# Optimization experiments

Hardware: AMD Instinct MI355X
Metric: run time of the kernel (lower is better)

The kernel has to match this reference:

```python
import jax, jax.numpy as jnp
import numpy as np

P, F, FR = 288, 7, 12      # time slots per day, days per week, sampling frequency scale
CHEB_K = 2
HID = 64


def _ste(time_index, SE, W_se, b_se, T_tod, T_dow):
    """Spatio-temporal embedding: learned spatial embedding projected to et_dim,
    plus time-of-day and day-of-week temporal embeddings. -> [B, N, et]"""
    t = time_index * FR
    tod = T_tod[t % P]                 # [B, et]
    dow = T_dow[(t // P) % F]          # [B, et]
    se = SE @ W_se + b_se              # [N, et]
    return se[None, :, :] + (tod + dow)[:, None, :]


def _avwgcn(x, STE, R, SC, Wpool, bpool):
    """Adaptive-vertex-weight graph conv (AGCRN-style) with dynamic STE-driven
    adjacency blended with dynamic relation R and static correlation SC.
    x: [B,N,Cin], STE: [B,N,et], R: [B,N,N], SC: [N,N]."""
    A = jax.nn.softmax(
        jax.nn.relu(jnp.einsum('bnd,bmd->bnm', STE, STE)) + R + SC[None], axis=-1)
    # Chebyshev polynomial supports applied to x (T0 = I handled implicitly)
    xs = [x, jnp.einsum('bnm,bmc->bnc', A, x)]
    for _ in range(CHEB_K - 2):
        xs.append(2.0 * jnp.einsum('bnm,bmc->bnc', A, xs[-1]) - xs[-2])
    x_g = jnp.stack(xs, axis=2)                        # [B,N,K,Cin]
    # per-node adaptive weights: W_n = STE @ Wpool; contracted without
    # materializing the [B,N,K,Cin,Cout] tensor
    g = jnp.einsum('bnki,dkio->bndo', x_g, Wpool)      # [B,N,et,Cout]
    out = jnp.einsum('bndo,bnd->bno', g, STE) + jnp.einsum('bnd,do->bno', STE, bpool)
    return out


def setup_inputs() -> dict:
    key = jax.random.key(0)
    ks = jax.random.split(key, 12)
    B, N, Din, et, es = 32, 1024, 1, 16, 16
    std = 0.1
    return {
        "x": jax.random.normal(ks[0], (B, N, Din), jnp.float32),
        "R": jax.random.normal(ks[1], (B, N, N), jnp.float32) * std,
        "state": jax.random.normal(ks[2], (B, N, HID), jnp.float32),
        "SC": jax.random.normal(ks[3], (N, N), jnp.float32) * std,
        "SE": jax.random.normal(ks[4], (N, es), jnp.float32),
        "W_se": jax.random.normal(ks[5], (es, et), jnp.float32) * std,
        "b_se": jnp.zeros((et,), jnp.float32),
        "T_tod": jax.random.normal(ks[6], (P, et), jnp.float32) * std,
        "T_dow": jax.random.normal(ks[7], (F, et), jnp.float32) * std,
        "W_gate": jax.random.normal(ks[8], (et, CHEB_K, Din + HID, 2 * HID), jnp.float32) * std,
        "b_gate": jnp.zeros((et, 2 * HID), jnp.float32),
        "W_upd": jax.random.normal(ks[9], (et, CHEB_K, Din + HID, HID), jnp.float32) * std,
        "b_upd": jnp.zeros((et, HID), jnp.float32),
        "time_index": jax.random.randint(ks[10], (B,), 0, P * F),
    }


def reference(x, R, state, SC, SE, W_se, b_se, T_tod, T_dow,
              W_gate, b_gate, W_upd, b_upd, time_index):
    STE = _ste(time_index, SE, W_se, b_se, T_tod, T_dow)       # [B,N,et]
    ins = jnp.concatenate([x, state], axis=-1)                 # [B,N,Din+H]
    z_r = jax.nn.sigmoid(_avwgcn(ins, STE, R, SC, W_gate, b_gate))
    z, r = jnp.split(z_r, 2, axis=-1)                          # each [B,N,H]
    cand = jnp.concatenate([x, z * state], axis=-1)
    hc = jnp.tanh(_avwgcn(cand, STE, R, SC, W_upd, b_upd))
    return r * state + (1.0 - r) * hc                          # [B,N,H]
```

## Files before the change

### kernel.cpp

```cpp
#include <hip/hip_runtime.h>
#include <math.h>

namespace {
constexpr int BB = 32;
constexpr int NN = 1024;
constexpr int ET = 16;
constexpr int HH = 64;
constexpr int CIN = 65;
constexpr int KI = 2*CIN;
constexpr int COG = 2*HH;
constexpr int COU = HH;
constexpr int PP = 288;
constexpr int FF = 7;
constexpr int FRQ = 12;
constexpr int XK = 160;

typedef __attribute__((ext_vector_type(4))) float f32x4;
typedef __attribute__((ext_vector_type(8))) short s16x8;
typedef __attribute__((ext_vector_type(4))) unsigned int u32x4;
typedef unsigned long long ull;

__device__ __forceinline__ float bf2f(unsigned short u) {
    unsigned v = ((unsigned)u) << 16;
    return __builtin_bit_cast(float, v);
}
__device__ __forceinline__ unsigned short f2bf(float f) {
    unsigned u = __builtin_bit_cast(unsigned, f);
    u += 0x7fffu + ((u >> 16) & 1u);
    return (unsigned short)(u >> 16);
}
__device__ __forceinline__ unsigned cvtpk(float lo, float hi) {
    unsigned r;
    asm("v_cvt_pk_bf16_f32 %0, %1, %2" : "=v"(r) : "v"(lo), "v"(hi));
    return r;
}
__device__ __forceinline__ float ldany(const float* p) { return *p; }
__device__ __forceinline__ float ldany(const unsigned short* p) { return bf2f(*p); }

__global__ void k_prep1(const float* __restrict__ SE, const float* __restrict__ Wse,
                        const float* __restrict__ bse, const float* __restrict__ Ttod,
                        const float* __restrict__ Tdow, const int* __restrict__ tidx,
                        float* __restrict__ se, float* __restrict__ tt) {
    int idx = blockIdx.x*blockDim.x + threadIdx.x;
    if (idx < NN*ET) {
        int n = idx / ET, d = idx % ET;
        float acc = bse[d];
        #pragma unroll
        for (int e = 0; e < ET; ++e) acc += SE[n*ET + e]*Wse[e*ET + d];
        se[idx] = acc;
    } else if (idx < NN*ET + BB*ET) {
        int r = idx - NN*ET;
        int b = r / ET, d = r % ET;
        int t = tidx[b]*FRQ;
        tt[r] = Ttod[(t % PP)*ET + d] + Tdow[((t/PP) % FF)*ET + d];
    }
}

__global__ void k_prep2(const float* __restrict__ se, const float* __restrict__ tt,
                        const float* __restrict__ Wg, const float* __restrict__ Wu,
                        unsigned short* __restrict__ stebf,
                        unsigned short* __restrict__ Wptg, unsigned short* __restrict__ Wptu) {
    int idx = blockIdx.x*blockDim.x + threadIdx.x;
    if (idx < BB*NN*ET) {
        int d = idx % ET;
        int n = (idx/ET) % NN;
        int b = idx/(ET*NN);
        stebf[idx] = f2bf(se[n*ET+d] + tt[b*ET+d]);
        return;
    }
    idx -= BB*NN*ET;
    if (idx < ET*COG*XK) {
        int d = idx/(COG*XK), r = idx%(COG*XK), o = r/XK, ki = r%XK;
        float v = (ki < KI) ? Wg[((size_t)d*KI + ki)*COG + o] : 0.f;
        Wptg[((size_t)d*COG + o)*XK + ki] = f2bf(v);
        return;
    }
    idx -= ET*COG*XK;
    if (idx < ET*COU*XK) {
        int d = idx/(COU*XK), r = idx%(COU*XK), o = r/XK, ki = r%XK;
        float v = (ki < KI) ? Wu[((size_t)d*KI + ki)*COU + o] : 0.f;
        Wptu[((size_t)d*COU + o)*XK + ki] = f2bf(v);
    }
}

template<typename T>
__global__ void k_vin(const float* __restrict__ x, const T* __restrict__ sv,
                      unsigned short* __restrict__ xgbf, unsigned short* __restrict__ vt) {
    int idx = blockIdx.x*blockDim.x + threadIdx.x;
    if (idx < BB*128*64) {
        int och = idx & 63, mb = (idx >> 6) & 127, b = idx >> 13;
        const T* src = sv + ((size_t)b*NN + mb*8)*HH + och;
        float v0=ldany(src), v1=ldany(src+HH), v2=ldany(src+2*HH), v3=ldany(src+3*HH);
        float v4=ldany(src+4*HH), v5=ldany(src+5*HH), v6=ldany(src+6*HH), v7=ldany(src+7*HH);
        ull lo = (ull)f2bf(v0) | ((ull)f2bf(v1)<<16) | ((ull)f2bf(v2)<<32) | ((ull)f2bf(v3)<<48);
        ull hi = (ull)f2bf(v4) | ((ull)f2bf(v5)<<16) | ((ull)f2bf(v6)<<32) | ((ull)f2bf(v7)<<48);
        ull* dst = (ull*)(vt + (size_t)idx*8);
        dst[0] = lo; dst[1] = hi;
        return;
    }
    idx -= BB*128*64;
    if (idx >= BB*NN*(XK/2)) return;
    int row = idx/(XK/2), c = idx%(XK/2);
    if (c < 32) {
        int k0 = 2*c;
        float v0 = (k0 == 0) ? x[row] : ldany(sv + (size_t)row*HH + k0 - 1);
        float v1 = ldany(sv + (size_t)row*HH + k0);
        ((unsigned*)xgbf)[(size_t)row*(XK/2) + c] = ((unsigned)f2bf(v1) << 16) | f2bf(v0);
    } else if (c == 32) {
        xgbf[(size_t)row*XK + 64] = f2bf(ldany(sv + (size_t)row*HH + 63));
    } else if (c >= 65) {
        ((unsigned*)xgbf)[(size_t)row*(XK/2) + c] = 0;
    }
}

constexpr int SSTR   = 1048;
constexpr int S_OFF  = 0;
constexpr int XV_OFF = 33536;
constexpr int MSH_OFF  = 37632;
constexpr int MSHC_OFF = 37888;
constexpr int LP_OFF   = 37952;
constexpr int AXP_OFF  = 38208;
constexpr int LSH_OFF  = 38464;
constexpr int SMEM_BYTES = 38528;

template<int PASS>
__global__ __launch_bounds__(256, 4) void k_attn(
    const unsigned short* __restrict__ stebf, const float* __restrict__ Rg,
    const float* __restrict__ SCg, const float* __restrict__ xg,
    const unsigned short* __restrict__ vt,
    float* __restrict__ Mr, float* __restrict__ Li,
    unsigned short* __restrict__ xgout, unsigned short* __restrict__ pglob)
{
    extern __shared__ char smem[];
    const int t = threadIdx.x, lane = t & 63, w = t >> 6;
    const int c15 = lane & 15, g = lane >> 4;
    const int strip = blockIdx.x, b = blockIdx.y;
    const size_t bN = (size_t)b * NN;
    const int r0 = strip * 16;

    float* Mshf  = (float*)(smem + MSH_OFF);
    float* MshCf = (float*)(smem + MSHC_OFF);
    float* Lshf  = (float*)(smem + LSH_OFF);

    if (PASS == 1) {
        ((float4*)(smem + XV_OFF))[t] = ((const float4*)(xg + bN))[t];
    } else {
        if (t < 16) Lshf[t] = Li[bN + r0 + t];
    }
    float mp2 = 0.f;
    if (PASS == 2) mp2 = Mr[bN + r0 + c15];

    float mx = -INFINITY;
    {
        s16x8 bfr = {0,0,0,0,0,0,0,0};
        if (g < 2) bfr = *(const s16x8*)(stebf + (bN + r0 + c15)*ET + g*8);
        const float* Rb  = Rg  + (bN + r0 + c15)*NN;
        const float* SCb = SCg + (size_t)(r0 + c15)*NN;
        const int colq = w*16 + g*4;
        s16x8 af0 = {0,0,0,0,0,0,0,0}, af1 = {0,0,0,0,0,0,0,0};
        if (g < 2) {
            af0 = *(const s16x8*)(stebf + (bN + 0*64 + w*16 + c15)*ET + g*8);
            af1 = *(const s16x8*)(stebf + (bN + 1*64 + w*16 + c15)*ET + g*8);
        }
        float4 rc0 = *(const float4*)(Rb + colq);
        float4 sc0 = *(const float4*)(SCb + colq);
        float4 rc1 = *(const float4*)(Rb + colq + 64);
        float4 sc1 = *(const float4*)(SCb + colq + 64);
        #pragma unroll
        for (int j = 0; j < 16; ++j) {
            s16x8 afc = af0; af0 = af1;
            float4 rcc = rc0, scc = sc0;
            rc0 = rc1; sc0 = sc1;
            if (j < 14) {
                if (g < 2) af1 = *(const s16x8*)(stebf + (bN + (j+2)*64 + w*16 + c15)*ET + g*8);
                rc1 = *(const float4*)(Rb + colq + (j+2)*64);
                sc1 = *(const float4*)(SCb + colq + (j+2)*64);
            }
            f32x4 zero = {0.f,0.f,0.f,0.f};
            f32x4 d = __builtin_amdgcn_mfma_f32_16x16x32_bf16(afc, bfr, zero, 0, 0, 0);
            float s0 = fmaxf(d[0],0.f) + rcc.x + scc.x;
            float s1 = fmaxf(d[1],0.f) + rcc.y + scc.y;
            float s2 = fmaxf(d[2],0.f) + rcc.z + scc.z;
            float s3 = fmaxf(d[3],0.f) + rcc.w + scc.w;
            unsigned byteo = (unsigned)(c15*SSTR + j*64 + colq)*2u;
            if (PASS == 1) {
                mx = fmaxf(mx, fmaxf(fmaxf(s0,s1), fmaxf(s2,s3)));
                *(ull*)(smem + S_OFF + byteo) = (ull)cvtpk(s0,s1) | ((ull)cvtpk(s2,s3) << 32);
            } else {
                float p0 = __expf(s0 - mp2), p1 = __expf(s1 - mp2);
                float p2 = __expf(s2 - mp2), p3 = __expf(s3 - mp2);
                *(ull*)(smem + S_OFF + byteo) = (ull)cvtpk(p0,p1) | ((ull)cvtpk(p2,p3) << 32);
            }
        }
    }

    if (PASS == 1) {
        mx = fmaxf(mx, __shfl_xor(mx, 16));
        mx = fmaxf(mx, __shfl_xor(mx, 32));
        if (lane < 16) Mshf[w*16 + c15] = mx;
        __syncthreads();
        if (t < 16) {
            float M = fmaxf(fmaxf(Mshf[t], Mshf[16+t]), fmaxf(Mshf[32+t], Mshf[48+t]));
            MshCf[t] = M;
            Mr[bN + r0 + t] = M;
        }
        __syncthreads();
        const int rowS = t >> 4, colblk = t & 15;
        const float m = MshCf[rowS];
        const size_t stripbase = ((size_t)b*64 + strip)*16384;
        float L = 0.f, ax = 0.f;
        #pragma unroll
        for (int i = 0; i < 8; ++i) {
            unsigned byteo = (unsigned)(rowS*SSTR + colblk*8 + i*128)*2u;
            s16x8 sv = *(const s16x8*)(smem + S_OFF + byteo);
            float p0 = __expf(bf2f((unsigned short)sv[0]) - m);
            float p1 = __expf(bf2f((unsigned short)sv[1]) - m);
            float p2 = __expf(bf2f((unsigned short)sv[2]) - m);
            float p3 = __expf(bf2f((unsigned short)sv[3]) - m);
            float p4 = __expf(bf2f((unsigned short)sv[4]) - m);
            float p5 = __expf(bf2f((unsigned short)sv[5]) - m);
            float p6 = __expf(bf2f((unsigned short)sv[6]) - m);
            float p7 = __expf(bf2f((unsigned short)sv[7]) - m);
            float4 xq0 = *(const float4*)(smem + XV_OFF + (unsigned)(colblk*8 + i*128)*4u);
            float4 xq1 = *(const float4*)(smem + XV_OFF + (unsigned)(colblk*8 + i*128 + 4)*4u);
            L += ((p0+p1)+(p2+p3)) + ((p4+p5)+(p6+p7));
            ax += p0*xq0.x + p1*xq0.y + p2*xq0.z + p3*xq0.w
                + p4*xq1.x + p5*xq1.y + p6*xq1.z + p7*xq1.w;
            u32x4 pw = { cvtpk(p0,p1), cvtpk(p2,p3), cvtpk(p4,p5), cvtpk(p6,p7) };
            *(u32x4*)(smem + S_OFF + byteo) = pw;
            if (pglob) {
                int cp = colblk + 16*i;
                *(u32x4*)(pglob + stripbase + (size_t)cp*128 + rowS*8) = pw;
            }
        }
        L += __shfl_xor(L, 1);  ax += __shfl_xor(ax, 1);
        L += __shfl_xor(L, 2);  ax += __shfl_xor(ax, 2);
        L += __shfl_xor(L, 4);  ax += __shfl_xor(ax, 4);
        L += __shfl_xor(L, 8);  ax += __shfl_xor(ax, 8);
        if ((lane & 15) == 0) {
            float li = 1.f / L;
            Lshf[rowS] = li;
            Li[bN + r0 + rowS] = li;
            xgout[(bN + r0 + rowS)*XK + 65] = f2bf(ax * li);
        }
        __syncthreads();
    } else {
        __syncthreads();
    }

    {
        f32x4 acc = {0.f,0.f,0.f,0.f};
        const unsigned short* vtb = vt + (size_t)b*65536 + (w*16 + c15)*8 + g*512;
        s16x8 bv0 = *(const s16x8*)(vtb);
        s16x8 bv1 = *(const s16x8*)(vtb + 2048);
        #pragma unroll
        for (int kk = 0; kk < 32; ++kk) {
            s16x8 bvc = bv0; bv0 = bv1;
            if (kk < 30) bv1 = *(const s16x8*)(vtb + (size_t)(kk+2)*2048);
            s16x8 a = *(const s16x8*)(smem + S_OFF + (unsigned)(c15*SSTR + kk*32 + g*8)*2u);
            acc = __builtin_amdgcn_mfma_f32_16x16x32_bf16(a, bvc, acc, 0, 0, 0);
        }
        #pragma unroll
        for (int q = 0; q < 4; ++q) {
            int rowl = g*4 + q;
            float li = Lshf[rowl];
            xgout[(bN + r0 + rowl)*XK + 66 + w*16 + c15] = f2bf(acc[q] * li);
        }
    }
}

__global__ __launch_bounds__(256, 4) void k_pv2(
    const unsigned short* __restrict__ pglob, const unsigned short* __restrict__ vt,
    const float* __restrict__ Li, unsigned short* __restrict__ xgout)
{
    const int t = threadIdx.x, lane = t & 63, w = t >> 6;
    const int c15 = lane & 15, g = lane >> 4;
    const int strip = blockIdx.x, b = blockIdx.y;
    const size_t bN = (size_t)b*NN;
    const int r0 = strip*16;

    const unsigned short* pA = pglob + ((size_t)b*64 + strip)*16384 + (size_t)lane*8;
    const unsigned short* pB = vt + (size_t)b*65536 + (w*16 + c15)*8 + g*512;

    f32x4 acc = {0.f,0.f,0.f,0.f};
    s16x8 a0 = *(const s16x8*)(pA);
    s16x8 b0 = *(const s16x8*)(pB);
    s16x8 a1 = *(const s16x8*)(pA + 512);
    s16x8 b1 = *(const s16x8*)(pB + 2048);
    #pragma unroll
    for (int kk = 0; kk < 32; ++kk) {
        s16x8 ac = a0, bc = b0;
        a0 = a1; b0 = b1;
        if (kk < 30) {
            a1 = *(const s16x8*)(pA + (size_t)(kk+2)*512);
            b1 = *(const s16x8*)(pB + (size_t)(kk+2)*2048);
        }
        acc = __builtin_amdgcn_mfma_f32_16x16x32_bf16(ac, bc, acc, 0, 0, 0);
    }
    #pragma unroll
    for (int q = 0; q < 4; ++q) {
        int row = r0 + g*4 + q;
        float li = Li[bN + row];
        xgout[(bN + row)*XK + 66 + w*16 + c15] = f2bf(acc[q]*li);
    }
}

template<int COUT, int EPI>
__global__ __launch_bounds__(256, 2) void k_apply(
    const unsigned short* __restrict__ Wpt, const float* __restrict__ bias,
    const unsigned short* __restrict__ stebf, const unsigned short* __restrict__ xgbf,
    const float* __restrict__ state, unsigned short* __restrict__ zsbf,
    unsigned short* __restrict__ rrbf, float* __restrict__ out)
{
    const int t = threadIdx.x, lane = t & 63, w = t >> 6;
    const int c15 = lane & 15, g = lane >> 4;
    const int n0 = blockIdx.x*32, b = blockIdx.y, oh = blockIdx.z;
    const int o = oh*64 + w*16 + c15;

    f32x4 acc[16][2];
    #pragma unroll
    for (int d = 0; d < 16; ++d) {
        acc[d][0] = (f32x4){0.f,0.f,0.f,0.f};
        acc[d][1] = (f32x4){0.f,0.f,0.f,0.f};
    }

    const unsigned short* Ar0 = xgbf + ((size_t)b*NN + n0 + c15)*XK + g*8;
    const unsigned short* Ar1 = Ar0 + (size_t)16*XK;
    const unsigned short* Bp  = Wpt + (size_t)o*XK + g*8;

    for (int ks = 0; ks < 5; ++ks) {
        s16x8 a0 = *(const s16x8*)(Ar0 + ks*32);
        s16x8 a1 = *(const s16x8*)(Ar1 + ks*32);
        #pragma unroll
        for (int d = 0; d < 16; ++d) {
            s16x8 bf = *(const s16x8*)(Bp + (size_t)d*COUT*XK + ks*32);
            acc[d][0] = __builtin_amdgcn_mfma_f32_16x16x32_bf16(a0, bf, acc[d][0], 0, 0, 0);
            acc[d][1] = __builtin_amdgcn_mfma_f32_16x16x32_bf16(a1, bf, acc[d][1], 0, 0, 0);
        }
    }

    float biasv[16];
    #pragma unroll
    for (int d = 0; d < 16; ++d) biasv[d] = bias[d*COUT + o];

    #pragma unroll
    for (int mt = 0; mt < 2; ++mt) {
        #pragma unroll
        for (int q = 0; q < 4; ++q) {
            int n = n0 + mt*16 + g*4 + q;
            size_t bn = (size_t)b*NN + n;
            const ull* sp = (const ull*)(stebf + bn*ET);
            float val = 0.f;
            #pragma unroll
            for (int dd = 0; dd < 4; ++dd) {
                ull sv4 = sp[dd];
                float s0 = bf2f((unsigned short)sv4);
                float s1 = bf2f((unsigned short)(sv4 >> 16));
                float s2 = bf2f((unsigned short)(sv4 >> 32));
                float s3 = bf2f((unsigned short)(sv4 >> 48));
                val += s0*(acc[dd*4+0][mt][q] + biasv[dd*4+0]);
                val += s1*(acc[dd*4+1][mt][q] + biasv[dd*4+1]);
                val += s2*(acc[dd*4+2][mt][q] + biasv[dd*4+2]);
                val += s3*(acc[dd*4+3][mt][q] + biasv[dd*4+3]);
            }
            if (EPI == 0) {
                float gv = 1.f/(1.f + __expf(-val));
                if (oh == 0) zsbf[bn*HH + o] = f2bf(gv * state[bn*HH + o]);
                else         rrbf[bn*HH + (o - 64)] = f2bf(gv);
            } else {
                float hc = tanhf(val);
                float rv = bf2f(rrbf[bn*HH + o]);
                out[bn*HH + o] = rv*state[bn*HH + o] + (1.f - rv)*hc;
            }
        }
    }
}

}

extern "C" void kernel_launch(void* const* d_in, const int* in_sizes, int n_in,
                              void* d_out, int out_size, void* d_ws, size_t ws_size,
                              hipStream_t stream) {
    const float* x     = (const float*)d_in[0];
    const float* R     = (const float*)d_in[1];
    const float* state = (const float*)d_in[2];
    const float* SC    = (const float*)d_in[3];
    const float* SE    = (const float*)d_in[4];
    const float* W_se  = (const float*)d_in[5];
    const float* b_se  = (const float*)d_in[6];
    const float* T_tod = (const float*)d_in[7];
    const float* T_dow = (const float*)d_in[8];
    const float* W_g   = (const float*)d_in[9];
    const float* b_g   = (const float*)d_in[10];
    const float* W_u   = (const float*)d_in[11];
    const float* b_u   = (const float*)d_in[12];
    const int*   tidx  = (const int*)d_in[13];
    float* out = (float*)d_out;
    float* ws = (float*)d_ws;

    float* se = ws;
    float* tt = se + 16384;
    float* Mr = tt + 512;
    float* Li = Mr + 32768;
    unsigned short* stebf = (unsigned short*)(Li + 32768);
    unsigned short* xgbf  = stebf + 524288;
    unsigned short* zsbf  = xgbf + 5242880;
    unsigned short* rrbf  = zsbf + 2097152;
    unsigned short* vt    = rrbf + 2097152;
    unsigned short* Wptg  = vt + 2097152;
    unsigned short* Wptu  = Wptg + 327680;
    unsigned short* pglob = Wptu + 163840;
    size_t need_bytes = (size_t)((char*)(pglob + 33554432) - (char*)ws);
    const bool haveP = ws_size >= need_bytes;

    k_prep1<<<66, 256, 0, stream>>>(SE, W_se, b_se, T_tod, T_dow, tidx, se, tt);
    k_prep2<<<3968, 256, 0, stream>>>(se, tt, W_g, W_u, stebf, Wptg, Wptu);

    k_vin<float><<<11264, 256, 0, stream>>>(x, state, xgbf, vt);
    k_attn<1><<<dim3(64, 32), 256, SMEM_BYTES, stream>>>(
        stebf, R, SC, x, vt, Mr, Li, xgbf, haveP ? pglob : nullptr);
    k_apply<COG, 0><<<dim3(32, 32, 2), 256, 0, stream>>>(
        Wptg, b_g, stebf, xgbf, state, zsbf, rrbf, nullptr);

    k_vin<unsigned short><<<11264, 256, 0, stream>>>(x, zsbf, xgbf, vt);
    if (haveP) {
        k_pv2<<<dim3(64, 32), 256, 0, stream>>>(pglob, vt, Li, xgbf);
    } else {
        k_attn<2><<<dim3(64, 32), 256, SMEM_BYTES, stream>>>(
            stebf, R, SC, x, vt, Mr, Li, xgbf, nullptr);
    }
    k_apply<COU, 1><<<dim3(32, 32, 1), 256, 0, stream>>>(
        Wptu, b_u, stebf, xgbf, state, zsbf, rrbf, out);
}
```

Measured before the change: 251.0 us.

## Split attention into register-resident score kernel plus separate PV matmul kernel

The first-pass attention kernel is replaced by k_score, which keeps the bf16-packed scores in registers instead of a large shared-memory tile. It computes the row max, exp, row sums and the x-column product, and writes the probability matrix P straight to global memory. The fused PV matmul from pass one moves to a separate k_pv2 launch, which also serves the second gate. The workspace-size fallback path is removed. This cuts shared memory so more blocks can run per CU (launch bounds raised to 5), at the cost of an extra kernel launch, re-reading P from global, more registers, and assuming the workspace is always large enough.

```diff
diff --git a/kernel.cpp b/kernel.cpp
--- a/kernel.cpp
+++ b/kernel.cpp
@@ -17,7 +17,6 @@
 
 typedef __attribute__((ext_vector_type(4))) float f32x4;
 typedef __attribute__((ext_vector_type(8))) short s16x8;
-typedef __attribute__((ext_vector_type(4))) unsigned int u32x4;
 typedef unsigned long long ull;
 
 __device__ __forceinline__ float bf2f(unsigned short u) {
@@ -113,50 +112,33 @@
     }
 }
 
-constexpr int SSTR   = 1048;
-constexpr int S_OFF  = 0;
-constexpr int XV_OFF = 33536;
-constexpr int MSH_OFF  = 37632;
-constexpr int MSHC_OFF = 37888;
-constexpr int LP_OFF   = 37952;
-constexpr int AXP_OFF  = 38208;
-constexpr int LSH_OFF  = 38464;
-constexpr int SMEM_BYTES = 38528;
-
-template<int PASS>
-__global__ __launch_bounds__(256, 4) void k_attn(
+__global__ __launch_bounds__(256, 5) void k_score(
     const unsigned short* __restrict__ stebf, const float* __restrict__ Rg,
     const float* __restrict__ SCg, const float* __restrict__ xg,
-    const unsigned short* __restrict__ vt,
-    float* __restrict__ Mr, float* __restrict__ Li,
-    unsigned short* __restrict__ xgout, unsigned short* __restrict__ pglob)
+    float* __restrict__ Li, unsigned short* __restrict__ xgout,
+    unsigned short* __restrict__ pglob)
 {
-    extern __shared__ char smem[];
+    __shared__ float XV[1024];
+    __shared__ float Mshf[64];
+    __shared__ float MshCf[16];
+    __shared__ float Lpf[64];
+    __shared__ float Axpf[64];
     const int t = threadIdx.x, lane = t & 63, w = t >> 6;
     const int c15 = lane & 15, g = lane >> 4;
     const int strip = blockIdx.x, b = blockIdx.y;
     const size_t bN = (size_t)b * NN;
     const int r0 = strip * 16;
-
-    float* Mshf  = (float*)(smem + MSH_OFF);
-    float* MshCf = (float*)(smem + MSHC_OFF);
-    float* Lshf  = (float*)(smem + LSH_OFF);
-
-    if (PASS == 1) {
-        ((float4*)(smem + XV_OFF))[t] = ((const float4*)(xg + bN))[t];
-    } else {
-        if (t < 16) Lshf[t] = Li[bN + r0 + t];
-    }
-    float mp2 = 0.f;
-    if (PASS == 2) mp2 = Mr[bN + r0 + c15];
-
+    const int colq = w*16 + g*4;
+
+    ((float4*)XV)[t] = ((const float4*)(xg + bN))[t];
+
+    unsigned spk[32];
     float mx = -INFINITY;
     {
         s16x8 bfr = {0,0,0,0,0,0,0,0};
         if (g < 2) bfr = *(const s16x8*)(stebf + (bN + r0 + c15)*ET + g*8);
         const float* Rb  = Rg  + (bN + r0 + c15)*NN;
         const float* SCb = SCg + (size_t)(r0 + c15)*NN;
-        const int colq = w*16 + g*4;
         s16x8 af0 = {0,0,0,0,0,0,0,0}, af1 = {0,0,0,0,0,0,0,0};
         if (g < 2) {
             af0 = *(const s16x8*)(stebf + (bN + 0*64 + w*16 + c15)*ET + g*8);
@@ -182,90 +164,48 @@
             float s1 = fmaxf(d[1],0.f) + rcc.y + scc.y;
             float s2 = fmaxf(d[2],0.f) + rcc.z + scc.z;
             float s3 = fmaxf(d[3],0.f) + rcc.w + scc.w;
-            unsigned byteo = (unsigned)(c15*SSTR + j*64 + colq)*2u;
-            if (PASS == 1) {
-                mx = fmaxf(mx, fmaxf(fmaxf(s0,s1), fmaxf(s2,s3)));
-                *(ull*)(smem + S_OFF + byteo) = (ull)cvtpk(s0,s1) | ((ull)cvtpk(s2,s3) << 32);
-            } else {
-                float p0 = __expf(s0 - mp2), p1 = __expf(s1 - mp2);
-                float p2 = __expf(s2 - mp2), p3 = __expf(s3 - mp2);
-                *(ull*)(smem + S_OFF + byteo) = (ull)cvtpk(p0,p1) | ((ull)cvtpk(p2,p3) << 32);
-            }
-        }
-    }
-
-    if (PASS == 1) {
-        mx = fmaxf(mx, __shfl_xor(mx, 16));
-        mx = fmaxf(mx, __shfl_xor(mx, 32));
-        if (lane < 16) Mshf[w*16 + c15] = mx;
-        __syncthreads();
-        if (t < 16) {
-            float M = fmaxf(fmaxf(Mshf[t], Mshf[16+t]), fmaxf(Mshf[32+t], Mshf[48+t]));
-            MshCf[t] = M;
-            Mr[bN + r0 + t] = M;
-        }
-        __syncthreads();
-        const int rowS = t >> 4, colblk = t & 15;
-        const float m = MshCf[rowS];
+            mx = fmaxf(mx, fmaxf(fmaxf(s0,s1), fmaxf(s2,s3)));
+            spk[2*j]   = cvtpk(s0, s1);
+            spk[2*j+1] = cvtpk(s2, s3);
+        }
+    }
+
+    mx = fmaxf(mx, __shfl_xor(mx, 16));
+    mx = fmaxf(mx, __shfl_xor(mx, 32));
+    if (lane < 16) Mshf[w*16 + c15] = mx;
+    __syncthreads();
+    if (t < 16) MshCf[t] = fmaxf(fmaxf(Mshf[t], Mshf[16+t]), fmaxf(Mshf[32+t], Mshf[48+t]));
+    __syncthreads();
+
+    {
+        const float m = MshCf[c15];
         const size_t stripbase = ((size_t)b*64 + strip)*16384;
         float L = 0.f, ax = 0.f;
         #pragma unroll
-        for (int i = 0; i < 8; ++i) {
-            unsigned byteo = (unsigned)(rowS*SSTR + colblk*8 + i*128)*2u;
-            s16x8 sv = *(const s16x8*)(smem + S_OFF + byteo);
-            float p0 = __expf(bf2f((unsigned short)sv[0]) - m);
-            float p1 = __expf(bf2f((unsigned short)sv[1]) - m);
-            float p2 = __expf(bf2f((unsigned short)sv[2]) - m);
-            float p3 = __expf(bf2f((unsigned short)sv[3]) - m);
-            float p4 = __expf(bf2f((unsigned short)sv[4]) - m);
-            float p5 = __expf(bf2f((unsigned short)sv[5]) - m);
-            float p6 = __expf(bf2f((unsigned short)sv[6]) - m);
-            float p7 = __expf(bf2f((unsigned short)sv[7]) - m);
-            float4 xq0 = *(const float4*)(smem + XV_OFF + (unsigned)(colblk*8 + i*128)*4u);
-            float4 xq1 = *(const float4*)(smem + XV_OFF + (unsigned)(colblk*8 + i*128 + 4)*4u);
-            L += ((p0+p1)+(p2+p3)) + ((p4+p5)+(p6+p7));
-            ax += p0*xq0.x + p1*xq0.y + p2*xq0.z + p3*xq0.w
-                + p4*xq1.x + p5*xq1.y + p6*xq1.z + p7*xq1.w;
-            u32x4 pw = { cvtpk(p0,p1), cvtpk(p2,p3), cvtpk(p4,p5), cvtpk(p6,p7) };
-            *(u32x4*)(smem + S_OFF + byteo) = pw;
-            if (pglob) {
-                int cp = colblk + 16*i;
-                *(u32x4*)(pglob + stripbase + (size_t)cp*128 + rowS*8) = pw;
-            }
-        }
-        L += __shfl_xor(L, 1);  ax += __shfl_xor(ax, 1);
-        L += __shfl_xor(L, 2);  ax += __shfl_xor(ax, 2);
-        L += __shfl_xor(L, 4);  ax += __shfl_xor(ax, 4);
-        L += __shfl_xor(L, 8);  ax += __shfl_xor(ax, 8);
-        if ((lane & 15) == 0) {
-            float li = 1.f / L;
-            Lshf[rowS] = li;
-            Li[bN + r0 + rowS] = li;
-            xgout[(bN + r0 + rowS)*XK + 65] = f2bf(ax * li);
-        }
-        __syncthreads();
-    } else {
-        __syncthreads();
-    }
-
-    {
-        f32x4 acc = {0.f,0.f,0.f,0.f};
-        const unsigned short* vtb = vt + (size_t)b*65536 + (w*16 + c15)*8 + g*512;
-        s16x8 bv0 = *(const s16x8*)(vtb);
-        s16x8 bv1 = *(const s16x8*)(vtb + 2048);
-        #pragma unroll
-        for (int kk = 0; kk < 32; ++kk) {
-            s16x8 bvc = bv0; bv0 = bv1;
-            if (kk < 30) bv1 = *(const s16x8*)(vtb + (size_t)(kk+2)*2048);
-            s16x8 a = *(const s16x8*)(smem + S_OFF + (unsigned)(c15*SSTR + kk*32 + g*8)*2u);
-            acc = __builtin_amdgcn_mfma_f32_16x16x32_bf16(a, bvc, acc, 0, 0, 0);
-        }
-        #pragma unroll
-        for (int q = 0; q < 4; ++q) {
-            int rowl = g*4 + q;
-            float li = Lshf[rowl];
-            xgout[(bN + r0 + rowl)*XK + 66 + w*16 + c15] = f2bf(acc[q] * li);
-        }
+        for (int j = 0; j < 16; ++j) {
+            unsigned u0 = spk[2*j], u1 = spk[2*j+1];
+            float p0 = __expf(bf2f((unsigned short)u0) - m);
+            float p1 = __expf(bf2f((unsigned short)(u0 >> 16)) - m);
+            float p2 = __expf(bf2f((unsigned short)u1) - m);
+            float p3 = __expf(bf2f((unsigned short)(u1 >> 16)) - m);
+            float4 xq = *(const float4*)(XV + j*64 + colq);
+            L += (p0 + p1) + (p2 + p3);
+            ax += p0*xq.x + p1*xq.y + p2*xq.z + p3*xq.w;
+            int cp = 8*j + 2*w + (g >> 1);
+            *(ull*)(pglob + stripbase + (size_t)cp*128 + c15*8 + (g & 1)*4) =
+                (ull)cvtpk(p0,p1) | ((ull)cvtpk(p2,p3) << 32);
+        }
+        L += __shfl_xor(L, 16);  ax += __shfl_xor(ax, 16);
+        L += __shfl_xor(L, 32);  ax += __shfl_xor(ax, 32);
+        if (lane < 16) { Lpf[w*16 + c15] = L; Axpf[w*16 + c15] = ax; }
+    }
+    __syncthreads();
+    if (t < 16) {
+        float Lt = Lpf[t] + Lpf[16+t] + Lpf[32+t] + Lpf[48+t];
+        float li = 1.f / Lt;
+        Li[bN + r0 + t] = li;
+        float axt = Axpf[t] + Axpf[16+t] + Axpf[32+t] + Axpf[48+t];
+        xgout[(bN + r0 + t)*XK + 65] = f2bf(axt * li);
     }
 }
 
@@ -410,25 +350,18 @@
     unsigned short* Wptg  = vt + 2097152;
     unsigned short* Wptu  = Wptg + 327680;
     unsigned short* pglob = Wptu + 163840;
-    size_t need_bytes = (size_t)((char*)(pglob + 33554432) - (char*)ws);
-    const bool haveP = ws_size >= need_bytes;
 
     k_prep1<<<66, 256, 0, stream>>>(SE, W_se, b_se, T_tod, T_dow, tidx, se, tt);
     k_prep2<<<3968, 256, 0, stream>>>(se, tt, W_g, W_u, stebf, Wptg, Wptu);
 
     k_vin<float><<<11264, 256, 0, stream>>>(x, state, xgbf, vt);
-    k_attn<1><<<dim3(64, 32), 256, SMEM_BYTES, stream>>>(
-        stebf, R, SC, x, vt, Mr, Li, xgbf, haveP ? pglob : nullptr);
+    k_score<<<dim3(64, 32), 256, 0, stream>>>(stebf, R, SC, x, Li, xgbf, pglob);
+    k_pv2<<<dim3(64, 32), 256, 0, stream>>>(pglob, vt, Li, xgbf);
     k_apply<COG, 0><<<dim3(32, 32, 2), 256, 0, stream>>>(
         Wptg, b_g, stebf, xgbf, state, zsbf, rrbf, nullptr);
 
     k_vin<unsigned short><<<11264, 256, 0, stream>>>(x, zsbf, xgbf, vt);
-    if (haveP) {
-        k_pv2<<<dim3(64, 32), 256, 0, stream>>>(pglob, vt, Li, xgbf);
-    } else {
-        k_attn<2><<<dim3(64, 32), 256, SMEM_BYTES, stream>>>(
-            stebf, R, SC, x, vt, Mr, Li, xgbf, nullptr);
-    }
+    k_pv2<<<dim3(64, 32), 256, 0, stream>>>(pglob, vt, Li, xgbf);
     k_apply<COU, 1><<<dim3(32, 32, 1), 256, 0, stream>>>(
         Wptu, b_u, stebf, xgbf, state, zsbf, rrbf, out);
 }
```

After: 274.3 us. +9.3%, slower.
